# Kernel optimization log

Measured on AMD Instinct MI355X. Metric: run time of the kernel, lower is better.

## Reference

```python
import jax, jax.numpy as jnp
import numpy as np

EMB = 1024
HEAD = 64

def setup_inputs() -> dict:
    key = jax.random.key(0)
    kx, kq, kk, kv = jax.random.split(key, 4)
    x = jax.random.normal(kx, (8, 2048, EMB), dtype=jnp.float32)
    # nn.Linear(emb, head, bias=False): y = x @ W.T, W: [head, emb]. Store as [emb, head].
    s = 1.0 / np.sqrt(EMB)
    Wq = jax.random.uniform(kq, (EMB, HEAD), jnp.float32, -s, s)
    Wk = jax.random.uniform(kk, (EMB, HEAD), jnp.float32, -s, s)
    Wv = jax.random.uniform(kv, (EMB, HEAD), jnp.float32, -s, s)
    return {"x": x, "Wq": Wq, "Wk": Wk, "Wv": Wv}

def reference(x, Wq, Wk, Wv):
    B, T, C = x.shape
    q = x @ Wq  # [B,T,H]
    k = x @ Wk
    v = x @ Wv
    # NOTE: original scales by emb_size C, not head_size.
    wei = jnp.einsum('bth,bsh->bts', q, k) / jnp.sqrt(jnp.asarray(C, x.dtype))
    causal = jnp.tril(jnp.ones((T, T), dtype=bool))
    wei = jnp.where(causal, wei, -jnp.inf)
    wei = jax.nn.softmax(wei, axis=-1)
    return jnp.einsum('bts,bsh->bth', wei, v)
```

## Files before the change

kernel.cpp:

```cpp
#include <hip/hip_runtime.h>
#include <hip/hip_bf16.h>

typedef __bf16 bf16_t;
typedef __bf16 bf16x8 __attribute__((ext_vector_type(8)));
typedef __bf16 bf16x4 __attribute__((ext_vector_type(4)));
typedef float  f32x4  __attribute__((ext_vector_type(4)));

#define MFMA_BF16(A, B, C) __builtin_amdgcn_mfma_f32_16x16x32_bf16((A), (B), (C), 0, 0, 0)

#define BATCH 8
#define SEQ   2048
#define EMB   1024
#define HEAD  64

typedef __attribute__((address_space(3))) void as3_void;
typedef const __attribute__((address_space(1))) void as1_void;
#define GLOAD_LDS16(g, l) \
  __builtin_amdgcn_global_load_lds((as1_void*)(g), (as3_void*)(l), 16, 0, 0)

__global__ __launch_bounds__(256) void wtrans_kernel(
    const float* __restrict__ Wq, const float* __restrict__ Wk,
    const float* __restrict__ Wv, bf16_t* __restrict__ WT)
{
  __shared__ float tile[64][65];
  const int m  = blockIdx.x >> 4;
  const int kt = blockIdx.x & 15;
  const float* W = (m == 0) ? Wq : (m == 1) ? Wk : Wv;
  const float scale = (m == 0) ? 0.045084219f : 1.0f;
  const int k0 = kt * 64;

  #pragma unroll
  for (int i = 0; i < 16; ++i) {
    int idx = i * 256 + threadIdx.x;
    int kk = idx >> 6, n = idx & 63;
    tile[kk][n] = W[(size_t)(k0 + kk) * HEAD + n];
  }
  __syncthreads();
  #pragma unroll
  for (int i = 0; i < 16; ++i) {
    int idx = i * 256 + threadIdx.x;
    int n = idx >> 6, kk = idx & 63;
    WT[((size_t)m * HEAD + n) * EMB + k0 + kk] = (bf16_t)(tile[kk][n] * scale);
  }
}

#define A_BYTES 16384
#define B_BYTES 24576
#define BUF_BYTES 40960

__global__ __launch_bounds__(512, 1) void qkv_kernel(
    const float* __restrict__ x, const bf16_t* __restrict__ WT,
    bf16_t* __restrict__ qo, bf16_t* __restrict__ ko, bf16_t* __restrict__ vT)
{
  __shared__ char lds[4 * BUF_BYTES];

  const int tid  = threadIdx.x;
  const int lane = tid & 63;
  const int wave = tid >> 6;
  const int l15 = lane & 15, l4 = lane >> 4;
  const int wm = wave >> 2, wn = wave & 3;
  const int rowbase = blockIdx.x * 64;
  const int phase = (blockIdx.x >> 3) & 15;

  const int a_rsub = lane >> 4;
  const int b_rsub = lane >> 3;
  const int b_koff = ((lane & 7) * 16) ^ (b_rsub << 4);

  const int aswz = (l15 & 7) << 5;
  const int bswz = (l15 & 7) << 4;

  f32x4 acc[2][3];
  #pragma unroll
  for (int m = 0; m < 2; ++m)
    #pragma unroll
    for (int n = 0; n < 3; ++n) acc[m][n] = (f32x4){0.f, 0.f, 0.f, 0.f};

#define STAGE(t)                                                               \
  {                                                                            \
    char* buf = lds + ((t) & 3) * BUF_BYTES;                                   \
    const int tp = ((t) + phase) & 15;                                         \
    _Pragma("unroll")                                                          \
    for (int j = 0; j < 2; ++j) {                                              \
      const int g = 2 * wave + j;                                              \
      const int koff = (l15 * 16) ^ ((((j) << 2) | a_rsub) << 5);              \
      const char* src = (const char*)x + (size_t)(rowbase + 4 * g + a_rsub)    \
                        * 4096 + (size_t)tp * 256 + koff;                      \
      GLOAD_LDS16(src, buf + g * 1024);                                        \
    }                                                                          \
    _Pragma("unroll")                                                          \
    for (int j = 0; j < 3; ++j) {                                              \
      const int g = 3 * wave + j;                                              \
      const char* src = (const char*)WT + (size_t)(8 * g + b_rsub) * 2048      \
                        + (size_t)tp * 128 + b_koff;                           \
      GLOAD_LDS16(src, buf + A_BYTES + g * 1024);                              \
    }                                                                          \
  }

#define COMPUTE(t)                                                             \
  {                                                                            \
    const char* Ab = lds + ((t) & 3) * BUF_BYTES;                              \
    const char* Bb = Ab + A_BYTES;                                             \
    _Pragma("unroll")                                                          \
    for (int ks = 0; ks < 2; ++ks) {                                           \
      bf16x8 afr[2];                                                           \
      _Pragma("unroll")                                                        \
      for (int m = 0; m < 2; ++m) {                                            \
        const int R = wm * 32 + m * 16 + l15;                                  \
        const char* rp = Ab + R * 256 + ((ks * 128 + l4 * 32) ^ aswz);         \
        f32x4 p0 = *(const f32x4*)(rp);                                        \
        f32x4 p1 = *(const f32x4*)(rp + 16);                                   \
        bf16x8 a;                                                              \
        a[0] = (bf16_t)p0.x; a[1] = (bf16_t)p0.y;                              \
        a[2] = (bf16_t)p0.z; a[3] = (bf16_t)p0.w;                              \
        a[4] = (bf16_t)p1.x; a[5] = (bf16_t)p1.y;                              \
        a[6] = (bf16_t)p1.z; a[7] = (bf16_t)p1.w;                              \
        afr[m] = a;                                                            \
      }                                                                        \
      _Pragma("unroll")                                                        \
      for (int n = 0; n < 3; ++n) {                                            \
        const int Rb = wn * 48 + n * 16 + l15;                                 \
        bf16x8 b = *(const bf16x8*)(Bb + Rb * 128 + ((ks * 64 + l4 * 16) ^ bswz)); \
        acc[0][n] = MFMA_BF16(afr[0], b, acc[0][n]);                           \
        acc[1][n] = MFMA_BF16(afr[1], b, acc[1][n]);                           \
      }                                                                        \
    }                                                                          \
  }

  STAGE(0); STAGE(1); STAGE(2);
  asm volatile("s_waitcnt vmcnt(10)" ::: "memory");
  __builtin_amdgcn_s_barrier();

  for (int t = 0; t < 13; ++t) {
    COMPUTE(t);
    STAGE(t + 3);
    asm volatile("s_waitcnt vmcnt(10)" ::: "memory");
    __builtin_amdgcn_s_barrier();
  }
  COMPUTE(13);
  asm volatile("s_waitcnt vmcnt(5)" ::: "memory");
  __builtin_amdgcn_s_barrier();
  COMPUTE(14);
  asm volatile("s_waitcnt vmcnt(0)" ::: "memory");
  __builtin_amdgcn_s_barrier();
  COMPUTE(15);
#undef STAGE
#undef COMPUTE

  #pragma unroll
  for (int n = 0; n < 3; ++n) {
    const int col = wn * 48 + n * 16;
    #pragma unroll
    for (int m = 0; m < 2; ++m) {
      const int r0 = rowbase + wm * 32 + m * 16 + l4 * 4;
      if (col < 64) {
        #pragma unroll
        for (int i = 0; i < 4; ++i)
          qo[(size_t)(r0 + i) * HEAD + col + l15] = (bf16_t)acc[m][n][i];
      } else if (col < 128) {
        #pragma unroll
        for (int i = 0; i < 4; ++i)
          ko[(size_t)(r0 + i) * HEAD + col - 64 + l15] = (bf16_t)acc[m][n][i];
      } else {
        const int h = col - 128 + l15;
        bf16x4 pk;
        #pragma unroll
        for (int i = 0; i < 4; ++i) pk[i] = (bf16_t)acc[m][n][i];
        *(bf16x4*)(vT + ((size_t)(r0 >> 11) * HEAD + h) * SEQ + (r0 & 2047)) = pk;
      }
    }
  }
}

__global__ __launch_bounds__(512, 2) void attn_kernel(
    const bf16_t* __restrict__ q, const bf16_t* __restrict__ k,
    const bf16_t* __restrict__ vT, float* __restrict__ out)
{
  __shared__ bf16_t P[8][16][72];
  __shared__ float olds[8][16][68];
  __shared__ float lsums[8][16];
  const int lane = threadIdx.x & 63;
  const int wave = threadIdx.x >> 6;
  const int l15 = lane & 15, l4 = lane >> 4;
  const int batch = blockIdx.x & 7;
  const int pair  = blockIdx.x >> 3;
  const int stripA = pair, stripB = 127 - pair;
  const int nA = (stripA >> 2) + 1;
  const int nB = (stripB >> 2) + 1;
  const int ntot = nA + nB;

  const bf16_t* kb = k  + (size_t)batch * SEQ * HEAD;
  const bf16_t* vb = vT + (size_t)batch * HEAD * SEQ;
  const bf16_t* qbA = q + ((size_t)batch * SEQ + stripA * 16) * HEAD;
  const bf16_t* qbB = q + ((size_t)batch * SEQ + stripB * 16) * HEAD;

  const bf16x8 aqA0 = *(const bf16x8*)(qbA + (size_t)l15 * HEAD + l4 * 8);
  const bf16x8 aqA1 = *(const bf16x8*)(qbA + (size_t)l15 * HEAD + 32 + l4 * 8);
  const bf16x8 aqB0 = *(const bf16x8*)(qbB + (size_t)l15 * HEAD + l4 * 8);
  const bf16x8 aqB1 = *(const bf16x8*)(qbB + (size_t)l15 * HEAD + 32 + l4 * 8);

  f32x4 oA[4], oB[4];
  #pragma unroll
  for (int i = 0; i < 4; ++i) {
    oA[i] = (f32x4){0.f, 0.f, 0.f, 0.f};
    oB[i] = (f32x4){0.f, 0.f, 0.f, 0.f};
  }
  float lsA[4] = {0.f, 0.f, 0.f, 0.f};
  float lsB[4] = {0.f, 0.f, 0.f, 0.f};

  const int cw  = (ntot - wave + 7) >> 3;
  const int ph  = pair;
  const int phm = ph - (ph / cw) * cw;

  for (int c = 0; c < cw; ++c) {
    int idx = c + phm; if (idx >= cw) idx -= cw;
    const int i = wave + (idx << 3);

    const bool isA = (i < nA);
    const int tile = isA ? i : (i - nA);
    const int nS   = isA ? nA : nB;
    const int qrow = (isA ? stripA : stripB) * 16;
    const int kv0  = tile * 64;
    const bf16x8 aq0 = isA ? aqA0 : aqB0;
    const bf16x8 aq1 = isA ? aqA1 : aqB1;

    f32x4 s[4];
    #pragma unroll
    for (int nf = 0; nf < 4; ++nf) s[nf] = (f32x4){0.f, 0.f, 0.f, 0.f};
    __builtin_amdgcn_s_setprio(1);
    #pragma unroll
    for (int nf = 0; nf < 4; ++nf) {
      const bf16_t* kp = kb + (size_t)(kv0 + nf * 16 + l15) * HEAD + l4 * 8;
      bf16x8 b0 = *(const bf16x8*)kp;
      bf16x8 b1 = *(const bf16x8*)(kp + 32);
      s[nf] = MFMA_BF16(aq0, b0, s[nf]);
      s[nf] = MFMA_BF16(aq1, b1, s[nf]);
    }
    __builtin_amdgcn_s_setprio(0);

    const bool diag = (tile == nS - 1);
    float tsum[4] = {0.f, 0.f, 0.f, 0.f};
    #pragma unroll
    for (int nf = 0; nf < 4; ++nf) {
      #pragma unroll
      for (int i2 = 0; i2 < 4; ++i2) {
        float e = exp2f(s[nf][i2]);
        if (diag) {
          const int col = kv0 + nf * 16 + l15;
          const int row = qrow + l4 * 4 + i2;
          e = (col <= row) ? e : 0.f;
        }
        tsum[i2] += e;
        P[wave][l4 * 4 + i2][nf * 16 + l15] = (bf16_t)e;
      }
    }

    bf16x8 v0[4], v1[4];
    #pragma unroll
    for (int nf = 0; nf < 4; ++nf) {
      const bf16_t* vp = vb + (size_t)(nf * 16 + l15) * SEQ + kv0 + l4 * 8;
      v0[nf] = *(const bf16x8*)vp;
      v1[nf] = *(const bf16x8*)(vp + 32);
    }
    asm volatile("s_waitcnt lgkmcnt(0)" ::: "memory");

    bf16x8 ap0 = *(const bf16x8*)&P[wave][l15][l4 * 8];
    bf16x8 ap1 = *(const bf16x8*)&P[wave][l15][32 + l4 * 8];
    __builtin_amdgcn_s_setprio(1);
    if (isA) {
      #pragma unroll
      for (int nf = 0; nf < 4; ++nf) {
        oA[nf] = MFMA_BF16(ap0, v0[nf], oA[nf]);
        oA[nf] = MFMA_BF16(ap1, v1[nf], oA[nf]);
      }
      #pragma unroll
      for (int i2 = 0; i2 < 4; ++i2) lsA[i2] += tsum[i2];
    } else {
      #pragma unroll
      for (int nf = 0; nf < 4; ++nf) {
        oB[nf] = MFMA_BF16(ap0, v0[nf], oB[nf]);
        oB[nf] = MFMA_BF16(ap1, v1[nf], oB[nf]);
      }
      #pragma unroll
      for (int i2 = 0; i2 < 4; ++i2) lsB[i2] += tsum[i2];
    }
    __builtin_amdgcn_s_setprio(0);
  }

  #pragma unroll
  for (int pass = 0; pass < 2; ++pass) {
    #pragma unroll
    for (int i = 0; i < 4; ++i) {
      float v = pass == 0 ? lsA[i] : lsB[i];
      v += __shfl_xor(v, 1);
      v += __shfl_xor(v, 2);
      v += __shfl_xor(v, 4);
      v += __shfl_xor(v, 8);
      if (l15 == 0) lsums[wave][l4 * 4 + i] = v;
    }
    #pragma unroll
    for (int nf = 0; nf < 4; ++nf)
      #pragma unroll
      for (int i = 0; i < 4; ++i)
        olds[wave][l4 * 4 + i][nf * 16 + l15] = pass == 0 ? oA[nf][i] : oB[nf][i];
    __syncthreads();

    if (threadIdx.x < 256) {
      const int r = threadIdx.x >> 4, c0 = threadIdx.x & 15;
      float sum = 0.f;
      #pragma unroll
      for (int w = 0; w < 8; ++w) sum += lsums[w][r];
      const float rinv = 1.0f / sum;
      const int strip = pass == 0 ? stripA : stripB;
      float* ob = out + ((size_t)batch * SEQ + strip * 16 + r) * HEAD;
      #pragma unroll
      for (int j = 0; j < 4; ++j) {
        const int c = c0 + 16 * j;
        float v = 0.f;
        #pragma unroll
        for (int w = 0; w < 8; ++w) v += olds[w][r][c];
        ob[c] = v * rinv;
      }
    }
    __syncthreads();
  }
}

extern "C" void kernel_launch(void* const* d_in, const int* in_sizes, int n_in,
                              void* d_out, int out_size, void* d_ws, size_t ws_size,
                              hipStream_t stream)
{
  const float* x  = (const float*)d_in[0];
  const float* Wq = (const float*)d_in[1];
  const float* Wk = (const float*)d_in[2];
  const float* Wv = (const float*)d_in[3];
  float* out = (float*)d_out;

  const size_t SZ_QKV = (size_t)BATCH * SEQ * HEAD * sizeof(bf16_t);
  if (ws_size < 3 * SZ_QKV + (size_t)192 * EMB * sizeof(bf16_t)) return;
  char* ws = (char*)d_ws;
  bf16_t* qo = (bf16_t*)(ws);
  bf16_t* ko = (bf16_t*)(ws + SZ_QKV);
  bf16_t* vT = (bf16_t*)(ws + 2 * SZ_QKV);
  bf16_t* WT = (bf16_t*)(ws + 3 * SZ_QKV);

  wtrans_kernel<<<dim3(48),  dim3(256), 0, stream>>>(Wq, Wk, Wv, WT);
  qkv_kernel  <<<dim3(256), dim3(512), 0, stream>>>(x, WT, qo, ko, vT);
  attn_kernel <<<dim3(512), dim3(512), 0, stream>>>(qo, ko, vT, out);
}
```

Measured before the change: 59.62 us.

## Split attention waves into two fixed groups per strip with single-pass reduction

Reworks the work split inside the attention block. Each group of 4 waves now owns one query strip of the mirrored pair and strides over that strip's KV tiles, replacing the 8-wave interleaving over the combined tile list with its rotating phase offset. This removes the per-tile isA branching, halves the accumulator registers, and lets the final reduction run in one pass across all 512 threads. The cost is load imbalance, since the long strip's group does far more tiles than the short strip's group. Launch bounds also drop to one block per SM, which reduces occupancy, and the olds padding changes to 65.

```diff
diff --git a/kernel.cpp b/kernel.cpp
--- a/kernel.cpp
+++ b/kernel.cpp
@@ -171,57 +171,38 @@
   }
 }
 
-__global__ __launch_bounds__(512, 2) void attn_kernel(
+__global__ __launch_bounds__(512, 1) void attn_kernel(
     const bf16_t* __restrict__ q, const bf16_t* __restrict__ k,
     const bf16_t* __restrict__ vT, float* __restrict__ out)
 {
   __shared__ bf16_t P[8][16][72];
-  __shared__ float olds[8][16][68];
+  __shared__ float olds[8][16][65];
   __shared__ float lsums[8][16];
   const int lane = threadIdx.x & 63;
   const int wave = threadIdx.x >> 6;
   const int l15 = lane & 15, l4 = lane >> 4;
   const int batch = blockIdx.x & 7;
   const int pair  = blockIdx.x >> 3;
-  const int stripA = pair, stripB = 127 - pair;
-  const int nA = (stripA >> 2) + 1;
-  const int nB = (stripB >> 2) + 1;
-  const int ntot = nA + nB;
+  const int side  = wave >> 2;
+  const int wsub  = wave & 3;
+  const int strip = side ? (127 - pair) : pair;
+  const int qrow  = strip * 16;
+  const int ntiles = (qrow >> 6) + 1;
 
   const bf16_t* kb = k  + (size_t)batch * SEQ * HEAD;
   const bf16_t* vb = vT + (size_t)batch * HEAD * SEQ;
-  const bf16_t* qbA = q + ((size_t)batch * SEQ + stripA * 16) * HEAD;
-  const bf16_t* qbB = q + ((size_t)batch * SEQ + stripB * 16) * HEAD;
-
-  const bf16x8 aqA0 = *(const bf16x8*)(qbA + (size_t)l15 * HEAD + l4 * 8);
-  const bf16x8 aqA1 = *(const bf16x8*)(qbA + (size_t)l15 * HEAD + 32 + l4 * 8);
-  const bf16x8 aqB0 = *(const bf16x8*)(qbB + (size_t)l15 * HEAD + l4 * 8);
-  const bf16x8 aqB1 = *(const bf16x8*)(qbB + (size_t)l15 * HEAD + 32 + l4 * 8);
-
-  f32x4 oA[4], oB[4];
-  #pragma unroll
-  for (int i = 0; i < 4; ++i) {
-    oA[i] = (f32x4){0.f, 0.f, 0.f, 0.f};
-    oB[i] = (f32x4){0.f, 0.f, 0.f, 0.f};
-  }
-  float lsA[4] = {0.f, 0.f, 0.f, 0.f};
-  float lsB[4] = {0.f, 0.f, 0.f, 0.f};
-
-  const int cw  = (ntot - wave + 7) >> 3;
-  const int ph  = pair;
-  const int phm = ph - (ph / cw) * cw;
-
-  for (int c = 0; c < cw; ++c) {
-    int idx = c + phm; if (idx >= cw) idx -= cw;
-    const int i = wave + (idx << 3);
-
-    const bool isA = (i < nA);
-    const int tile = isA ? i : (i - nA);
-    const int nS   = isA ? nA : nB;
-    const int qrow = (isA ? stripA : stripB) * 16;
-    const int kv0  = tile * 64;
-    const bf16x8 aq0 = isA ? aqA0 : aqB0;
-    const bf16x8 aq1 = isA ? aqA1 : aqB1;
+  const bf16_t* qb = q  + ((size_t)batch * SEQ + qrow) * HEAD;
+
+  const bf16x8 aq0 = *(const bf16x8*)(qb + (size_t)l15 * HEAD + l4 * 8);
+  const bf16x8 aq1 = *(const bf16x8*)(qb + (size_t)l15 * HEAD + 32 + l4 * 8);
+
+  f32x4 o[4];
+  #pragma unroll
+  for (int i = 0; i < 4; ++i) o[i] = (f32x4){0.f, 0.f, 0.f, 0.f};
+  float lsum[4] = {0.f, 0.f, 0.f, 0.f};
+
+  for (int t = wsub; t < ntiles; t += 4) {
+    const int kv0 = t * 64;
 
     f32x4 s[4];
     #pragma unroll
@@ -237,8 +218,7 @@
     }
     __builtin_amdgcn_s_setprio(0);
 
-    const bool diag = (tile == nS - 1);
-    float tsum[4] = {0.f, 0.f, 0.f, 0.f};
+    const bool diag = (t == ntiles - 1);
     #pragma unroll
     for (int nf = 0; nf < 4; ++nf) {
       #pragma unroll
@@ -249,7 +229,7 @@
           const int row = qrow + l4 * 4 + i2;
           e = (col <= row) ? e : 0.f;
         }
-        tsum[i2] += e;
+        lsum[i2] += e;
         P[wave][l4 * 4 + i2][nf * 16 + l15] = (bf16_t)e;
       }
     }
@@ -266,62 +246,45 @@
     bf16x8 ap0 = *(const bf16x8*)&P[wave][l15][l4 * 8];
     bf16x8 ap1 = *(const bf16x8*)&P[wave][l15][32 + l4 * 8];
     __builtin_amdgcn_s_setprio(1);
-    if (isA) {
-      #pragma unroll
-      for (int nf = 0; nf < 4; ++nf) {
-        oA[nf] = MFMA_BF16(ap0, v0[nf], oA[nf]);
-        oA[nf] = MFMA_BF16(ap1, v1[nf], oA[nf]);
-      }
-      #pragma unroll
-      for (int i2 = 0; i2 < 4; ++i2) lsA[i2] += tsum[i2];
-    } else {
-      #pragma unroll
-      for (int nf = 0; nf < 4; ++nf) {
-        oB[nf] = MFMA_BF16(ap0, v0[nf], oB[nf]);
-        oB[nf] = MFMA_BF16(ap1, v1[nf], oB[nf]);
-      }
-      #pragma unroll
-      for (int i2 = 0; i2 < 4; ++i2) lsB[i2] += tsum[i2];
+    #pragma unroll
+    for (int nf = 0; nf < 4; ++nf) {
+      o[nf] = MFMA_BF16(ap0, v0[nf], o[nf]);
+      o[nf] = MFMA_BF16(ap1, v1[nf], o[nf]);
     }
     __builtin_amdgcn_s_setprio(0);
   }
 
   #pragma unroll
-  for (int pass = 0; pass < 2; ++pass) {
-    #pragma unroll
-    for (int i = 0; i < 4; ++i) {
-      float v = pass == 0 ? lsA[i] : lsB[i];
-      v += __shfl_xor(v, 1);
-      v += __shfl_xor(v, 2);
-      v += __shfl_xor(v, 4);
-      v += __shfl_xor(v, 8);
-      if (l15 == 0) lsums[wave][l4 * 4 + i] = v;
-    }
-    #pragma unroll
-    for (int nf = 0; nf < 4; ++nf)
-      #pragma unroll
-      for (int i = 0; i < 4; ++i)
-        olds[wave][l4 * 4 + i][nf * 16 + l15] = pass == 0 ? oA[nf][i] : oB[nf][i];
-    __syncthreads();
-
-    if (threadIdx.x < 256) {
-      const int r = threadIdx.x >> 4, c0 = threadIdx.x & 15;
-      float sum = 0.f;
-      #pragma unroll
-      for (int w = 0; w < 8; ++w) sum += lsums[w][r];
-      const float rinv = 1.0f / sum;
-      const int strip = pass == 0 ? stripA : stripB;
-      float* ob = out + ((size_t)batch * SEQ + strip * 16 + r) * HEAD;
-      #pragma unroll
-      for (int j = 0; j < 4; ++j) {
-        const int c = c0 + 16 * j;
-        float v = 0.f;
-        #pragma unroll
-        for (int w = 0; w < 8; ++w) v += olds[w][r][c];
-        ob[c] = v * rinv;
-      }
-    }
-    __syncthreads();
+  for (int i = 0; i < 4; ++i) {
+    float v = lsum[i];
+    v += __shfl_xor(v, 1);
+    v += __shfl_xor(v, 2);
+    v += __shfl_xor(v, 4);
+    v += __shfl_xor(v, 8);
+    if (l15 == 0) lsums[wave][l4 * 4 + i] = v;
+  }
+  #pragma unroll
+  for (int nf = 0; nf < 4; ++nf)
+    #pragma unroll
+    for (int i = 0; i < 4; ++i)
+      olds[wave][l4 * 4 + i][nf * 16 + l15] = o[nf][i];
+  __syncthreads();
+
+  {
+    const int g  = threadIdx.x >> 8;
+    const int tt = threadIdx.x & 255;
+    const int r = tt >> 4, c0 = tt & 15;
+    const int sstrip = g ? (127 - pair) : pair;
+    const int w0 = g * 4;
+    const float s = lsums[w0][r] + lsums[w0+1][r] + lsums[w0+2][r] + lsums[w0+3][r];
+    const float rinv = 1.0f / s;
+    float* ob = out + ((size_t)batch * SEQ + sstrip * 16 + r) * HEAD;
+    #pragma unroll
+    for (int j = 0; j < 4; ++j) {
+      const int c = c0 + 16 * j;
+      float v = olds[w0][r][c] + olds[w0+1][r][c] + olds[w0+2][r][c] + olds[w0+3][r][c];
+      ob[c] = v * rinv;
+    }
   }
 }
 
```

After: 56.57 us. 1.05x faster.
